# Kernel tuning notes

Hardware: AMD Instinct MI355X
Metric: run time of the kernel (lower is better)

Reference implementation:

```python
import jax, jax.numpy as jnp
import numpy as np

RF = 3          # receptive_field_size (cubic)
STRIDE = 1
TEMP = 1.0      # softmax temperature ('soft' sampling, eval mode: no Gumbel noise)
TREE_DEPTH = 4

# Truth table of all 16 binary gates: GATES[g, t] = value of gate g on input
# pattern t = 2*a + b (a = first child, b = second child), t in {0,1,2,3}.
GATES = np.array([[(g >> t) & 1 for t in range(4)] for g in range(16)],
                 dtype=np.float32)  # (16, 4)


def _lut_eval(a, b, w):
    """Differentiable 2-input LUT. a, b: (B,K,P,nodes); w: (nodes,K,16)."""
    probs = jax.nn.softmax(w / TEMP, axis=-1)          # (nodes,K,16)
    lut = probs @ jnp.asarray(GATES)                   # (nodes,K,4) relaxed truth table
    lut = jnp.moveaxis(lut, 0, 1)[:, None]             # (K,1,nodes,4) -> bcast over B,P
    l0, l1, l2, l3 = lut[..., 0], lut[..., 1], lut[..., 2], lut[..., 3]
    na, nb = 1.0 - a, 1.0 - b
    # E[lut(a,b)] under independent Bernoulli inputs
    return l0 * na * nb + l1 * na * b + l2 * a * nb + l3 * a * b


def setup_inputs() -> dict:
    key = jax.random.key(0)
    ks = jax.random.split(key, 8)
    B, C, H, W, D = 4, 3, 32, 32, 32
    K, S = 32, 16  # num_kernels, lut_rank**tree_depth leaves
    x = jax.random.uniform(ks[0], (B, C, H, W, D), dtype=jnp.float32)
    # (lut_rank=2, K, S, 4) coords (h, w, d, c); rf=3 and channels=3 so all in [0,3)
    kernel_coords = jax.random.randint(ks[1], (2, K, S, 4), 0, 3, dtype=jnp.int32)
    w0 = jax.random.normal(ks[2], (16, K, 16), dtype=jnp.float32)
    w1 = jax.random.normal(ks[3], (8, K, 16), dtype=jnp.float32)
    w2 = jax.random.normal(ks[4], (4, K, 16), dtype=jnp.float32)
    w3 = jax.random.normal(ks[5], (2, K, 16), dtype=jnp.float32)
    w4 = jax.random.normal(ks[6], (1, K, 16), dtype=jnp.float32)
    return {"x": x, "kernel_coords": kernel_coords,
            "w0": w0, "w1": w1, "w2": w2, "w3": w3, "w4": w4}


def reference(x, kernel_coords, w0, w1, w2, w3, w4):
    B, C, H, W, D = x.shape
    OH, OW, OD = (H - RF) // STRIDE + 1, (W - RF) // STRIDE + 1, (D - RF) // STRIDE + 1
    kc = kernel_coords
    # linear offset of each leaf coord inside flattened (C,H,W,D) volume
    base = ((kc[..., 3] * H + kc[..., 0]) * W + kc[..., 1]) * D + kc[..., 2]  # (2,K,S)
    oh = jnp.arange(OH) * STRIDE
    ow = jnp.arange(OW) * STRIDE
    od = jnp.arange(OD) * STRIDE
    patch = ((oh[:, None, None] * W + ow[None, :, None]) * D
             + od[None, None, :]).reshape(-1)                                  # (P,)
    lin = base[:, :, None, :] + patch[None, None, :, None]                     # (2,K,P,S)
    g = x.reshape(B, -1)[:, lin]                                               # (B,2,K,P,S)
    out = _lut_eval(g[:, 0], g[:, 1], w0)                                      # (B,K,P,S)
    for w in (w1, w2, w3, w4):  # binary tree reduction over TREE_DEPTH levels
        out = _lut_eval(out[..., 0::2], out[..., 1::2], w)
    return out.reshape(B, out.shape[1], OH, OW, OD)
```

## Files before the change

### kernel.cpp

```cpp
#include <hip/hip_runtime.h>


#define B_  4
#define C_  3
#define H_  32
#define W_  32
#define D_  32
#define K_  32
#define S_  16
#define TPB 256
#define NX  393216

typedef float    v8f __attribute__((ext_vector_type(8)));
typedef _Float16 h8  __attribute__((ext_vector_type(8), aligned(16)));
typedef float    f4a __attribute__((ext_vector_type(4), aligned(4)));
typedef float    f2a __attribute__((ext_vector_type(2), aligned(4)));

__device__ __forceinline__ v8f cvt8(h8 h) {
    v8f r;
    #pragma unroll
    for (int i = 0; i < 8; ++i) r[i] = (float)h[i];
    return r;
}

__device__ __forceinline__ v8f lut8(v8f a, v8f b, float l0, float d1, float d2, float d3) {
    const v8f t0 = a * d2 + l0;
    const v8f t1 = a * d3 + d1;
    return b * t1 + t0;
}

__global__ __launch_bounds__(TPB) void prepass(const float* __restrict__ x,
                                               _Float16* __restrict__ y) {
    const int i = blockIdx.x * TPB + threadIdx.x;
    const int d = i & 31;
    const float v0 = x[i];
    const float v1 = (d < 31) ? x[i + 1] : 0.f;
    const float v2 = (d < 30) ? x[i + 2] : 0.f;
    y[i]          = (_Float16)v0;
    y[NX + i]     = (_Float16)v1;
    y[2 * NX + i] = (_Float16)v2;
}

__global__ __launch_bounds__(TPB, 4) void logic_conv3d(
    const _Float16* __restrict__ y,
    const int*      __restrict__ kc,
    const float*    __restrict__ w0,
    const float*    __restrict__ w1,
    const float*    __restrict__ w2,
    const float*    __restrict__ w3,
    const float*    __restrict__ w4,
    float*          __restrict__ out)
{
    __shared__ float4 s_lut[31];
    __shared__ int    s_lb[32];

    const int bk  = blockIdx.x;
    const int b   = bk >> 5;
    const int k   = bk & 31;
    const int tid = threadIdx.x;

    if (tid < 31) {
        const float* wp; int ln;
        if      (tid < 16) { wp = w0; ln = tid;      }
        else if (tid < 24) { wp = w1; ln = tid - 16; }
        else if (tid < 28) { wp = w2; ln = tid - 24; }
        else if (tid < 30) { wp = w3; ln = tid - 28; }
        else               { wp = w4; ln = 0;        }
        const float* wrow = wp + (ln * K_ + k) * 16;
        float lg[16];
        float m = -1e30f;
        #pragma unroll
        for (int g = 0; g < 16; ++g) { lg[g] = wrow[g]; m = fmaxf(m, lg[g]); }
        float z = 0.f;
        #pragma unroll
        for (int g = 0; g < 16; ++g) { lg[g] = __expf(lg[g] - m); z += lg[g]; }
        const float inv = 1.0f / z;
        float l0 = 0.f, l1 = 0.f, l2 = 0.f, l3 = 0.f;
        #pragma unroll
        for (int g = 0; g < 16; ++g) {
            float p = lg[g] * inv;
            if (g & 1) l0 += p;
            if (g & 2) l1 += p;
            if (g & 4) l2 += p;
            if (g & 8) l3 += p;
        }
        s_lut[tid] = make_float4(l0, l1 - l0, l2 - l0, (l3 - l2) - (l1 - l0));
    } else if (tid >= 32 && tid < 64) {
        const int idx  = tid - 32;
        const int tree = idx >> 4;
        const int s    = idx & 15;
        const int off  = ((tree * K_ + k) * S_ + s) * 4;
        const int h = kc[off + 0], w = kc[off + 1], d = kc[off + 2], c = kc[off + 3];
        s_lb[idx] = d * NX + ((c * H_ + h) * W_ + w) * D_;
    }
    __syncthreads();

    int sAB[32];
    #pragma unroll
    for (int i = 0; i < 8; ++i) {
        const int4 q = *(const int4*)&s_lb[i * 4];
        sAB[i * 4 + 0] = __builtin_amdgcn_readfirstlane(q.x);
        sAB[i * 4 + 1] = __builtin_amdgcn_readfirstlane(q.y);
        sAB[i * 4 + 2] = __builtin_amdgcn_readfirstlane(q.z);
        sAB[i * 4 + 3] = __builtin_amdgcn_readfirstlane(q.w);
    }

    const int ohl = tid >> 7;
    const int r   = tid & 127;
    const int ow  = r >> 2;
    const int gq  = r & 3;
    const int od0 = gq << 3;

    if (ow < 30) {
        const int oh   = blockIdx.y * 2 + ohl;
        const int voff = b * (C_ * H_ * W_ * D_) + oh * (W_ * D_) + ow * D_ + od0;

        v8f v1[8];
        #pragma unroll
        for (int j = 0; j < 8; ++j) {
            const int s0 = 2 * j, s1 = 2 * j + 1;
            const v8f A0 = cvt8(*(const h8*)(y + sAB[s0]      + voff));
            const v8f B0 = cvt8(*(const h8*)(y + sAB[16 + s0] + voff));
            const float4 L0 = s_lut[s0];
            const v8f t0 = lut8(A0, B0, L0.x, L0.y, L0.z, L0.w);
            const v8f A1 = cvt8(*(const h8*)(y + sAB[s1]      + voff));
            const v8f B1 = cvt8(*(const h8*)(y + sAB[16 + s1] + voff));
            const float4 L1 = s_lut[s1];
            const v8f t1 = lut8(A1, B1, L1.x, L1.y, L1.z, L1.w);
            const float4 LN = s_lut[16 + j];
            v1[j] = lut8(t0, t1, LN.x, LN.y, LN.z, LN.w);
        }

        #pragma unroll
        for (int j = 0; j < 4; ++j) {
            const float4 L = s_lut[24 + j];
            v1[j] = lut8(v1[2 * j], v1[2 * j + 1], L.x, L.y, L.z, L.w);
        }
        #pragma unroll
        for (int j = 0; j < 2; ++j) {
            const float4 L = s_lut[28 + j];
            v1[j] = lut8(v1[2 * j], v1[2 * j + 1], L.x, L.y, L.z, L.w);
        }
        {
            const float4 L = s_lut[30];
            v1[0] = lut8(v1[0], v1[1], L.x, L.y, L.z, L.w);
        }

        float* outp = out + (size_t)bk * 27000 + oh * 900 + ow * 30 + od0;
        f4a lo; lo[0] = v1[0][0]; lo[1] = v1[0][1]; lo[2] = v1[0][2]; lo[3] = v1[0][3];
        *(f4a*)outp = lo;
        if (gq < 3) {
            f4a hi; hi[0] = v1[0][4]; hi[1] = v1[0][5]; hi[2] = v1[0][6]; hi[3] = v1[0][7];
            *(f4a*)(outp + 4) = hi;
        } else {
            f2a hi2; hi2[0] = v1[0][4]; hi2[1] = v1[0][5];
            *(f2a*)(outp + 4) = hi2;
        }
    }
}

extern "C" void kernel_launch(void* const* d_in, const int* in_sizes, int n_in,
                              void* d_out, int out_size, void* d_ws, size_t ws_size,
                              hipStream_t stream) {
    const float* x  = (const float*)d_in[0];
    const int*   kc = (const int*)d_in[1];
    const float* w0 = (const float*)d_in[2];
    const float* w1 = (const float*)d_in[3];
    const float* w2 = (const float*)d_in[4];
    const float* w3 = (const float*)d_in[5];
    const float* w4 = (const float*)d_in[6];
    float* out = (float*)d_out;
    _Float16* y = (_Float16*)d_ws;

    prepass<<<NX / TPB, TPB, 0, stream>>>(x, y);
    dim3 grid(B_ * K_, 15);
    logic_conv3d<<<grid, TPB, 0, stream>>>(y, kc, w0, w1, w2, w3, w4, out);
}
```

Measured before the change: 86.44 us.

## Stage fp32 input slab in LDS and serve 12 of 32 leaf gathers from it

```diff
diff --git a/kernel.cpp b/kernel.cpp
--- a/kernel.cpp
+++ b/kernel.cpp
@@ -8,10 +8,13 @@
 #define D_  32
 #define K_  32
 #define S_  16
+#define WS  33
 #define TPB 256
 #define NX  393216
+#define CHWD (C_ * H_ * W_ * D_)
 
 typedef float    v8f __attribute__((ext_vector_type(8)));
+typedef float    f8a __attribute__((ext_vector_type(8), aligned(4)));
 typedef _Float16 h8  __attribute__((ext_vector_type(8), aligned(16)));
 typedef float    f4a __attribute__((ext_vector_type(4), aligned(4)));
 typedef float    f2a __attribute__((ext_vector_type(2), aligned(4)));
@@ -41,7 +44,8 @@
     y[2 * NX + i] = (_Float16)v2;
 }
 
-__global__ __launch_bounds__(TPB, 4) void logic_conv3d(
+__global__ __launch_bounds__(TPB, 3) void logic_conv3d(
+    const float*    __restrict__ x,
     const _Float16* __restrict__ y,
     const int*      __restrict__ kc,
     const float*    __restrict__ w0,
@@ -52,7 +56,9 @@
     float*          __restrict__ out)
 {
     __shared__ float4 s_lut[31];
-    __shared__ int    s_lb[32];
+    __shared__ int    s_lb[16];
+    __shared__ int    s_gb[32];
+    __shared__ __align__(16) float slab[12 * 32 * WS + 8];
 
     const int bk  = blockIdx.x;
     const int b   = bk >> 5;
@@ -91,18 +97,41 @@
         const int s    = idx & 15;
         const int off  = ((tree * K_ + k) * S_ + s) * 4;
         const int h = kc[off + 0], w = kc[off + 1], d = kc[off + 2], c = kc[off + 3];
-        s_lb[idx] = d * NX + ((c * H_ + h) * W_ + w) * D_;
+        s_gb[idx] = d * NX + ((c * H_ + h) * W_ + w) * D_;
+        if (tree == 0)
+            s_lb[s] = ((c * 4 + h) * 32 + w) * WS + d;
+    }
+
+    {
+        const float* xb = x + (size_t)b * CHWD + (blockIdx.y * 2) * (W_ * D_);
+        const int w  = tid >> 3;
+        const int d4 = (tid & 7) << 2;
+        #pragma unroll
+        for (int it = 0; it < 12; ++it) {
+            const int c  = it >> 2;
+            const int dh = it & 3;
+            const float4 val = *(const float4*)(xb + c * (H_ * W_ * D_) + dh * (W_ * D_) + tid * 4);
+            *(float4*)&slab[((c * 4 + dh) * 32 + w) * WS + d4] = val;
+        }
     }
     __syncthreads();
 
-    int sAB[32];
+    int sL[12], sG[32];
+    #pragma unroll
+    for (int i = 0; i < 3; ++i) {
+        const int4 q = *(const int4*)&s_lb[i * 4];
+        sL[i * 4 + 0] = __builtin_amdgcn_readfirstlane(q.x);
+        sL[i * 4 + 1] = __builtin_amdgcn_readfirstlane(q.y);
+        sL[i * 4 + 2] = __builtin_amdgcn_readfirstlane(q.z);
+        sL[i * 4 + 3] = __builtin_amdgcn_readfirstlane(q.w);
+    }
     #pragma unroll
     for (int i = 0; i < 8; ++i) {
-        const int4 q = *(const int4*)&s_lb[i * 4];
-        sAB[i * 4 + 0] = __builtin_amdgcn_readfirstlane(q.x);
-        sAB[i * 4 + 1] = __builtin_amdgcn_readfirstlane(q.y);
-        sAB[i * 4 + 2] = __builtin_amdgcn_readfirstlane(q.z);
-        sAB[i * 4 + 3] = __builtin_amdgcn_readfirstlane(q.w);
+        const int4 q = *(const int4*)&s_gb[i * 4];
+        sG[i * 4 + 0] = __builtin_amdgcn_readfirstlane(q.x);
+        sG[i * 4 + 1] = __builtin_amdgcn_readfirstlane(q.y);
+        sG[i * 4 + 2] = __builtin_amdgcn_readfirstlane(q.z);
+        sG[i * 4 + 3] = __builtin_amdgcn_readfirstlane(q.w);
     }
 
     const int ohl = tid >> 7;
@@ -112,19 +141,22 @@
     const int od0 = gq << 3;
 
     if (ow < 30) {
-        const int oh   = blockIdx.y * 2 + ohl;
-        const int voff = b * (C_ * H_ * W_ * D_) + oh * (W_ * D_) + ow * D_ + od0;
+        const int oh = blockIdx.y * 2 + ohl;
+        const int vs = ohl * (32 * WS) + ow * WS + od0;
+        const int vg = b * CHWD + oh * (W_ * D_) + ow * D_ + od0;
 
         v8f v1[8];
         #pragma unroll
         for (int j = 0; j < 8; ++j) {
             const int s0 = 2 * j, s1 = 2 * j + 1;
-            const v8f A0 = cvt8(*(const h8*)(y + sAB[s0]      + voff));
-            const v8f B0 = cvt8(*(const h8*)(y + sAB[16 + s0] + voff));
+            const v8f A0 = (s0 < 12) ? (v8f)(*(const f8a*)&slab[sL[s0] + vs])
+                                     : cvt8(*(const h8*)(y + sG[s0] + vg));
+            const v8f B0 = cvt8(*(const h8*)(y + sG[16 + s0] + vg));
             const float4 L0 = s_lut[s0];
             const v8f t0 = lut8(A0, B0, L0.x, L0.y, L0.z, L0.w);
-            const v8f A1 = cvt8(*(const h8*)(y + sAB[s1]      + voff));
-            const v8f B1 = cvt8(*(const h8*)(y + sAB[16 + s1] + voff));
+            const v8f A1 = (s1 < 12) ? (v8f)(*(const f8a*)&slab[sL[s1] + vs])
+                                     : cvt8(*(const h8*)(y + sG[s1] + vg));
+            const v8f B1 = cvt8(*(const h8*)(y + sG[16 + s1] + vg));
             const float4 L1 = s_lut[s1];
             const v8f t1 = lut8(A1, B1, L1.x, L1.y, L1.z, L1.w);
             const float4 LN = s_lut[16 + j];
@@ -174,5 +206,5 @@
 
     prepass<<<NX / TPB, TPB, 0, stream>>>(x, y);
     dim3 grid(B_ * K_, 15);
-    logic_conv3d<<<grid, TPB, 0, stream>>>(y, kc, w0, w1, w2, w3, w4, out);
-}
+    logic_conv3d<<<grid, TPB, 0, stream>>>(x, y, kc, w0, w1, w2, w3, w4, out);
+}
```

After: 88.41 us. 1.02x slower.
